# Kernel optimization log

Hardware: AMD Instinct MI355X
Metric: run time of the kernel (lower is better)

The kernel has to match this reference:

```python
import jax, jax.numpy as jnp
import numpy as np

B, T, V = 512, 200, 2048
E, H, I, A = 20, 100, 64, 32  # embedding, hidden, intermediate, actions


def setup_inputs() -> dict:
    key = jax.random.key(0)
    ks = jax.random.split(key, 12)
    batch = jax.random.uniform(ks[0], (B, T, V), dtype=jnp.float32)
    lengths = jax.random.randint(ks[1], (B,), 1, T + 1)
    s = 0.05
    W_emb = jax.random.normal(ks[2], (E, V), dtype=jnp.float32) * s
    b_emb = jnp.zeros((E,), jnp.float32)
    W_ih = jax.random.normal(ks[3], (4 * H, E), dtype=jnp.float32) * s
    W_hh = jax.random.normal(ks[4], (4 * H, H), dtype=jnp.float32) * s
    b_ih = jnp.zeros((4 * H,), jnp.float32)
    # torch init sets forget-gate bias (second quarter) to 1.0 in bias_hh
    b_hh = jnp.zeros((4 * H,), jnp.float32).at[H:2 * H].set(1.0)
    W1 = jax.random.normal(ks[5], (I, H), dtype=jnp.float32) * s
    b1 = jnp.zeros((I,), jnp.float32)
    W2 = jax.random.normal(ks[6], (A, I), dtype=jnp.float32) * s
    b2 = jnp.zeros((A,), jnp.float32)
    h0 = jnp.zeros((B, H), jnp.float32)
    c0 = jnp.zeros((B, H), jnp.float32)
    return {"batch": batch, "lengths": lengths, "W_emb": W_emb, "b_emb": b_emb,
            "W_ih": W_ih, "W_hh": W_hh, "b_ih": b_ih, "b_hh": b_hh,
            "W1": W1, "b1": b1, "W2": W2, "b2": b2, "h0": h0, "c0": c0}


def reference(batch, lengths, W_emb, b_emb, W_ih, W_hh, b_ih, b_hh,
              W1, b1, W2, b2, h0, c0):
    # Embedding via Linear: [B,T,V] @ [V,E] -> [B,T,E]
    emb = jnp.einsum('btv,ev->bte', batch, W_emb) + b_emb
    # Precompute input contribution to all gates: [B,T,4H]
    xg = jnp.einsum('bte,ge->btg', emb, W_ih) + b_ih + b_hh

    def step(carry, xg_t):
        h, c = carry
        gates = xg_t + h @ W_hh.T  # [B,4H]
        i, f, g, o = jnp.split(gates, 4, axis=-1)  # torch gate order i,f,g,o
        c = jax.nn.sigmoid(f) * c + jax.nn.sigmoid(i) * jnp.tanh(g)
        h = jax.nn.sigmoid(o) * jnp.tanh(c)
        return (h, c), h

    _, ys = jax.lax.scan(step, (h0, c0), jnp.swapaxes(xg, 0, 1))  # ys: [T,B,H]
    nb = batch.shape[0]
    h_final = ys[lengths - 1, jnp.arange(nb)]  # [B,H] output at last valid step
    inter = jax.nn.relu(h_final @ W1.T + b1)
    actions = inter @ W2.T + b2
    return actions
```

## Files before the change

### kernel.cpp

```cpp
#include <hip/hip_runtime.h>

#define BB 512
#define TT 200
#define VV 2048
#define EE 20
#define HH 100
#define G4 400
#define II 64
#define AA 32

typedef float vf2 __attribute__((ext_vector_type(2)));

#define WS_WT_OFF  1024
#define WS_EMB_OFF (1024 + VV * EE)

__global__ __launch_bounds__(512) void k0_prep(
    const int* __restrict__ lengths, const float* __restrict__ W_emb,
    int* __restrict__ off, float* __restrict__ Wt)
{
    if (blockIdx.x == 0) {
        __shared__ int s[BB];
        int tid = threadIdx.x;
        s[tid] = lengths[tid];
        __syncthreads();
        for (int d = 1; d < BB; d <<= 1) {
            int v = (tid >= d) ? s[tid - d] : 0;
            __syncthreads();
            if (tid >= d) s[tid] += v;
            __syncthreads();
        }
        off[tid + 1] = s[tid];
        if (tid == 0) off[0] = 0;
    } else {
        int idx = (blockIdx.x - 1) * 512 + threadIdx.x;
        if (idx < VV * EE) {
            int k = idx / EE, e = idx - k * EE;
            Wt[idx] = W_emb[(size_t)e * VV + k];
        }
    }
}

#define R1   128
#define KC   64
#define TSTR 68

__global__ __launch_bounds__(128) void k1_embed(
    const float* __restrict__ batch, const int* __restrict__ off,
    const float* __restrict__ Wt, const float* __restrict__ b_emb,
    float* __restrict__ emb)
{
    __shared__ float tile[R1 * TSTR];
    __shared__ float wch[(KC / 2) * EE * 2];
    __shared__ int   roff[R1];

    const int tid  = threadIdx.x;
    const int Nv   = off[BB];
    const int row0 = blockIdx.x * R1;
    if (row0 >= Nv) return;

    const int row    = row0 + tid;
    const bool active = row < Nv;

    int b = 0;
    {
        const int r = active ? row : 0;
        int lo = 0, hi = BB;
        while (lo + 1 < hi) {
            int mid = (lo + hi) >> 1;
            if (off[mid] <= r) lo = mid; else hi = mid;
        }
        b = lo;
    }
    const int t = (active ? row : 0) - off[b];
    roff[tid] = b * TT + t;
    __syncthreads();

    const float* srcp[16];
#pragma unroll
    for (int i = 0; i < 16; ++i) {
        int r = (tid >> 4) + 8 * i;
        srcp[i] = batch + (size_t)roff[r] * VV + (tid & 15) * 4;
    }

    vf2 acc[EE];
#pragma unroll
    for (int e = 0; e < EE; ++e) { acc[e].x = 0.f; acc[e].y = 0.f; }

#pragma unroll 1
    for (int c0 = 0; c0 < VV; c0 += KC) {
        __syncthreads();
#pragma unroll
        for (int i = 0; i < 16; ++i) {
            int r = (tid >> 4) + 8 * i;
            float4 v = *reinterpret_cast<const float4*>(srcp[i] + c0);
            *reinterpret_cast<float4*>(&tile[r * TSTR + (tid & 15) * 4]) = v;
        }
#pragma unroll
        for (int i = 0; i < 10; ++i) {
            int l = tid + i * 128;
            int k = l / EE, e = l - k * EE;
            wch[(k >> 1) * (2 * EE) + e * 2 + (k & 1)] = Wt[(size_t)c0 * EE + l];
        }
        __syncthreads();
#pragma unroll
        for (int p = 0; p < 16; ++p) {
            float4 xv = *reinterpret_cast<const float4*>(&tile[tid * TSTR + p * 4]);
            vf2 xlo, xhi;
            xlo.x = xv.x; xlo.y = xv.y;
            xhi.x = xv.z; xhi.y = xv.w;
            const float* wlo = &wch[(2 * p) * (2 * EE)];
            const float* whi = &wch[(2 * p + 1) * (2 * EE)];
#pragma unroll
            for (int e2 = 0; e2 < EE / 2; ++e2) {
                float4 wv = *reinterpret_cast<const float4*>(wlo + e2 * 4);
                vf2 w0, w1;
                w0.x = wv.x; w0.y = wv.y;
                w1.x = wv.z; w1.y = wv.w;
                acc[2 * e2]     = __builtin_elementwise_fma(w0, xlo, acc[2 * e2]);
                acc[2 * e2 + 1] = __builtin_elementwise_fma(w1, xlo, acc[2 * e2 + 1]);
            }
#pragma unroll
            for (int e2 = 0; e2 < EE / 2; ++e2) {
                float4 wv = *reinterpret_cast<const float4*>(whi + e2 * 4);
                vf2 w0, w1;
                w0.x = wv.x; w0.y = wv.y;
                w1.x = wv.z; w1.y = wv.w;
                acc[2 * e2]     = __builtin_elementwise_fma(w0, xhi, acc[2 * e2]);
                acc[2 * e2 + 1] = __builtin_elementwise_fma(w1, xhi, acc[2 * e2 + 1]);
            }
        }
    }

    if (active) {
        float o[EE];
#pragma unroll
        for (int e = 0; e < EE; ++e) o[e] = acc[e].x + acc[e].y + b_emb[e];
        float* dst = emb + (size_t)(b * TT + t) * EE;
#pragma unroll
        for (int e = 0; e < EE; e += 4)
            *reinterpret_cast<float4*>(dst + e) = make_float4(o[e], o[e+1], o[e+2], o[e+3]);
    }
}

__device__ __forceinline__ float fast_sig(float x) { return 1.f / (1.f + __expf(-x)); }
__device__ __forceinline__ float fast_tanh(float x) {
    x = fminf(fmaxf(x, -15.f), 15.f);
    float e = __expf(2.f * x);
    return (e - 1.f) / (e + 1.f);
}
__device__ __forceinline__ float dpp_xor1_add(float v) {
    int p = __builtin_amdgcn_update_dpp(0, __builtin_bit_cast(int, v), 0xB1, 0xF, 0xF, true);
    return v + __builtin_bit_cast(float, p);
}
__device__ __forceinline__ float dpp_xor2_add(float v) {
    int p = __builtin_amdgcn_update_dpp(0, __builtin_bit_cast(int, v), 0x4E, 0xF, 0xF, true);
    return v + __builtin_bit_cast(float, p);
}
#define QSTR 36

__global__ __launch_bounds__(448) void k2_lstm(
    const float* __restrict__ emb, const int* __restrict__ lengths,
    const float* __restrict__ W_ih, const float* __restrict__ W_hh,
    const float* __restrict__ b_ih, const float* __restrict__ b_hh,
    const float* __restrict__ W1, const float* __restrict__ b1,
    const float* __restrict__ W2, const float* __restrict__ b2,
    const float* __restrict__ h0, const float* __restrict__ c0,
    float* __restrict__ out)
{
    __shared__ float xhbuf[2][2][160];
    __shared__ float hfin[2][HH];
    __shared__ float inter[2][II];

    const int tid = threadIdx.x;
    const int b0  = blockIdx.x * 2;
    const int len0 = lengths[b0];
    const int len1 = lengths[b0 + 1];
    const int tmax = (len0 > len1) ? len0 : len1;

    const int j = tid >> 2, q = tid & 3;

    for (int i = tid; i < 2 * 2 * 160; i += 448) (&xhbuf[0][0][0])[i] = 0.f;

    vf2 w2[4][16];
    float biasv[4];
    float c_reg = 0.f;
    int lenq = 0;
    if (tid < G4) {
        const int rr[4] = { j, HH + j, 2 * HH + j, 3 * HH + j };
#pragma unroll
        for (int g = 0; g < 4; ++g) {
            const int r = rr[g];
#pragma unroll
            for (int mp = 0; mp < 16; ++mp) {
                int k = q * 32 + mp * 2;
                float2 v;
                if (k + 1 < EE)          v = *reinterpret_cast<const float2*>(&W_ih[r * EE + k]);
                else if (k + 1 < EE + HH) v = *reinterpret_cast<const float2*>(&W_hh[r * HH + k - EE]);
                else                     v = make_float2(0.f, 0.f);
                w2[g][mp].x = v.x; w2[g][mp].y = v.y;
            }
            biasv[g] = b_ih[r] + b_hh[r];
        }
        if (q < 2) c_reg = c0[(size_t)(b0 + q) * HH + j];
        lenq = (q == 0) ? len0 : len1;
    }
    __syncthreads();

    float xreg = 0.f;
    if (tid < G4) {
        if (q < 2) {
            int i = EE + j;
            xhbuf[0][q][(i >> 5) * QSTR + (i & 31)] = h0[(size_t)(b0 + q) * HH + j];
        }
    } else if (tid < G4 + 2 * EE) {
        const int wdx = tid - G4, bw = wdx / EE, e = wdx - bw * EE;
        const float* ep = emb + (size_t)(b0 + bw) * TT * EE;
        xhbuf[0][bw][e] = ep[e];
        xreg = ep[EE + e];
    }
    __syncthreads();

#pragma unroll 1
    for (int t = 0; t < tmax; ++t) {
        const int cur = t & 1, nxt = cur ^ 1;
        if (tid < G4) {
            vf2 a[4][2];
#pragma unroll
            for (int g = 0; g < 4; ++g) { a[g][0].x=0.f; a[g][0].y=0.f; a[g][1].x=0.f; a[g][1].y=0.f; }
            const float* xc = &xhbuf[cur][0][0];
#pragma unroll
            for (int m8 = 0; m8 < 8; ++m8) {
                float4 x0 = *reinterpret_cast<const float4*>(xc + q * QSTR + m8 * 4);
                float4 x1 = *reinterpret_cast<const float4*>(xc + 160 + q * QSTR + m8 * 4);
                vf2 xl0, xh0, xl1, xh1;
                xl0.x = x0.x; xl0.y = x0.y;  xh0.x = x0.z; xh0.y = x0.w;
                xl1.x = x1.x; xl1.y = x1.y;  xh1.x = x1.z; xh1.y = x1.w;
#pragma unroll
                for (int g = 0; g < 4; ++g) {
                    a[g][0] = __builtin_elementwise_fma(w2[g][2*m8],   xl0, a[g][0]);
                    a[g][0] = __builtin_elementwise_fma(w2[g][2*m8+1], xh0, a[g][0]);
                    a[g][1] = __builtin_elementwise_fma(w2[g][2*m8],   xl1, a[g][1]);
                    a[g][1] = __builtin_elementwise_fma(w2[g][2*m8+1], xh1, a[g][1]);
                }
            }
            float s_[4][2];
#pragma unroll
            for (int g = 0; g < 4; ++g) {
#pragma unroll
                for (int bb = 0; bb < 2; ++bb) {
                    float v = a[g][bb].x + a[g][bb].y;
                    v = dpp_xor1_add(v);
                    v = dpp_xor2_add(v);
                    s_[g][bb] = v;
                }
            }
            if (q < 2) {
                float gi = s_[0][q] + biasv[0];
                float gf = s_[1][q] + biasv[1];
                float gg = s_[2][q] + biasv[2];
                float go = s_[3][q] + biasv[3];
                c_reg = fast_sig(gf) * c_reg + fast_sig(gi) * fast_tanh(gg);
                float hv = fast_sig(go) * fast_tanh(c_reg);
                int i = EE + j;
                xhbuf[nxt][q][(i >> 5) * QSTR + (i & 31)] = hv;
                if (t == lenq - 1) hfin[q][j] = hv;
            }
        } else if (tid < G4 + 2 * EE) {
            const int wdx = tid - G4, bw = wdx / EE, e = wdx - bw * EE;
            xhbuf[nxt][bw][e] = xreg;
            xreg = (t + 2 < TT)
                 ? emb[((size_t)(b0 + bw) * TT + (t + 2)) * EE + e] : 0.f;
        }
        __syncthreads();
    }

    if (tid < 2 * II) {
        int bb = tid >> 6, i = tid & 63;
        float a = b1[i];
        const float* w1r = W1 + i * HH;
#pragma unroll
        for (int k = 0; k < HH; k += 4) {
            a += w1r[k] * hfin[bb][k] + w1r[k+1] * hfin[bb][k+1]
               + w1r[k+2] * hfin[bb][k+2] + w1r[k+3] * hfin[bb][k+3];
        }
        inter[bb][i] = fmaxf(a, 0.f);
    }
    __syncthreads();
    if (tid < 2 * AA) {
        int bb = tid >> 5, ai = tid & 31;
        float a = b2[ai];
        const float* w2r = W2 + ai * II;
#pragma unroll
        for (int k = 0; k < II; ++k) a += w2r[k] * inter[bb][k];
        out[(size_t)(b0 + bb) * AA + ai] = a;
    }
}

extern "C" void kernel_launch(void* const* d_in, const int* in_sizes, int n_in,
                              void* d_out, int out_size, void* d_ws, size_t ws_size,
                              hipStream_t stream) {
    const float* batch  = (const float*)d_in[0];
    const int*   lengths= (const int*)  d_in[1];
    const float* W_emb  = (const float*)d_in[2];
    const float* b_emb  = (const float*)d_in[3];
    const float* W_ih   = (const float*)d_in[4];
    const float* W_hh   = (const float*)d_in[5];
    const float* b_ih   = (const float*)d_in[6];
    const float* b_hh   = (const float*)d_in[7];
    const float* W1     = (const float*)d_in[8];
    const float* b1     = (const float*)d_in[9];
    const float* W2     = (const float*)d_in[10];
    const float* b2     = (const float*)d_in[11];
    const float* h0     = (const float*)d_in[12];
    const float* c0     = (const float*)d_in[13];
    float* out = (float*)d_out;

    int*   off = (int*)d_ws;
    float* Wt  = (float*)d_ws + WS_WT_OFF;
    float* emb = (float*)d_ws + WS_EMB_OFF;

    k0_prep<<<1 + (VV * EE + 511) / 512, 512, 0, stream>>>(lengths, W_emb, off, Wt);
    k1_embed<<<(BB * TT + R1 - 1) / R1, R1, 0, stream>>>(batch, off, Wt, b_emb, emb);
    k2_lstm<<<BB / 2, 448, 0, stream>>>(emb, lengths, W_ih, W_hh, b_ih, b_hh,
                                        W1, b1, W2, b2, h0, c0, out);
}
```

Baseline: 445.3 us.

## Prefetch embedding tiles into registers, stage emb in LDS, spread gate activations across lanes

The embedding GEMM now loads the next K-chunk of batch rows and weights into registers while the current chunk is computed, replacing the load-then-sync pattern with a software-pipelined double-buffer. The LSTM kernel copies each block's whole embedding sequence into shared memory up front, so the per-step global emb loads go away. The gate nonlinearities are spread so each of the four lanes per hidden unit evaluates one gate activation, with the results exchanged via DPP moves. This lowers the serial per-step transcendental latency. The cost is more registers in the GEMM kernel and about 32KB of extra LDS per LSTM block, which may reduce occupancy.

Result: slower. 508.1 us (+14.1%).

```diff
diff --git a/kernel.cpp b/kernel.cpp
--- a/kernel.cpp
+++ b/kernel.cpp
@@ -86,22 +86,35 @@
 #pragma unroll
     for (int e = 0; e < EE; ++e) { acc[e].x = 0.f; acc[e].y = 0.f; }
 
+    float4 xr[16];
+    float  wr[10];
+#pragma unroll
+    for (int i = 0; i < 16; ++i) xr[i] = *reinterpret_cast<const float4*>(srcp[i]);
+#pragma unroll
+    for (int i = 0; i < 10; ++i) wr[i] = Wt[tid + i * 128];
+
 #pragma unroll 1
     for (int c0 = 0; c0 < VV; c0 += KC) {
-        __syncthreads();
 #pragma unroll
         for (int i = 0; i < 16; ++i) {
             int r = (tid >> 4) + 8 * i;
-            float4 v = *reinterpret_cast<const float4*>(srcp[i] + c0);
-            *reinterpret_cast<float4*>(&tile[r * TSTR + (tid & 15) * 4]) = v;
+            *reinterpret_cast<float4*>(&tile[r * TSTR + (tid & 15) * 4]) = xr[i];
         }
 #pragma unroll
         for (int i = 0; i < 10; ++i) {
             int l = tid + i * 128;
             int k = l / EE, e = l - k * EE;
-            wch[(k >> 1) * (2 * EE) + e * 2 + (k & 1)] = Wt[(size_t)c0 * EE + l];
+            wch[(k >> 1) * (2 * EE) + e * 2 + (k & 1)] = wr[i];
         }
         __syncthreads();
+        if (c0 + KC < VV) {
+#pragma unroll
+            for (int i = 0; i < 16; ++i)
+                xr[i] = *reinterpret_cast<const float4*>(srcp[i] + c0 + KC);
+#pragma unroll
+            for (int i = 0; i < 10; ++i)
+                wr[i] = Wt[(size_t)(c0 + KC) * EE + tid + i * 128];
+        }
 #pragma unroll
         for (int p = 0; p < 16; ++p) {
             float4 xv = *reinterpret_cast<const float4*>(&tile[tid * TSTR + p * 4]);
@@ -129,6 +142,7 @@
                 acc[2 * e2 + 1] = __builtin_elementwise_fma(w1, xhi, acc[2 * e2 + 1]);
             }
         }
+        __syncthreads();
     }
 
     if (active) {
@@ -155,6 +169,11 @@
 __device__ __forceinline__ float dpp_xor2_add(float v) {
     int p = __builtin_amdgcn_update_dpp(0, __builtin_bit_cast(int, v), 0x4E, 0xF, 0xF, true);
     return v + __builtin_bit_cast(float, p);
+}
+template<int CTRL>
+__device__ __forceinline__ float dpp_mov(float v) {
+    int p = __builtin_amdgcn_update_dpp(0, __builtin_bit_cast(int, v), CTRL, 0xF, 0xF, true);
+    return __builtin_bit_cast(float, p);
 }
 #define QSTR 36
 
@@ -167,6 +186,7 @@
     const float* __restrict__ h0, const float* __restrict__ c0,
     float* __restrict__ out)
 {
+    __shared__ float emb_lds[2][TT][EE];
     __shared__ float xhbuf[2][2][160];
     __shared__ float hfin[2][HH];
     __shared__ float inter[2][II];
@@ -176,10 +196,14 @@
     const int len0 = lengths[b0];
     const int len1 = lengths[b0 + 1];
     const int tmax = (len0 > len1) ? len0 : len1;
-
     const int j = tid >> 2, q = tid & 3;
 
     for (int i = tid; i < 2 * 2 * 160; i += 448) (&xhbuf[0][0][0])[i] = 0.f;
+    {
+        const float4* srcp = reinterpret_cast<const float4*>(emb + (size_t)b0 * TT * EE);
+        float4* dst = reinterpret_cast<float4*>(&emb_lds[0][0][0]);
+        for (int i = tid; i < 2 * TT * EE / 4; i += 448) dst[i] = srcp[i];
+    }
 
     vf2 w2[4][16];
     float biasv[4];
@@ -206,7 +230,6 @@
     }
     __syncthreads();
 
-    float xreg = 0.f;
     if (tid < G4) {
         if (q < 2) {
             int i = EE + j;
@@ -214,9 +237,7 @@
         }
     } else if (tid < G4 + 2 * EE) {
         const int wdx = tid - G4, bw = wdx / EE, e = wdx - bw * EE;
-        const float* ep = emb + (size_t)(b0 + bw) * TT * EE;
-        xhbuf[0][bw][e] = ep[e];
-        xreg = ep[EE + e];
+        xhbuf[0][bw][e] = emb_lds[bw][0][e];
     }
     __syncthreads();
 
@@ -254,22 +275,28 @@
                     s_[g][bb] = v;
                 }
             }
+            float vq0 = (q==0) ? s_[0][0] : (q==1) ? s_[1][0] : (q==2) ? s_[2][0] : s_[3][0];
+            float vq1 = (q==0) ? s_[0][1] : (q==1) ? s_[1][1] : (q==2) ? s_[2][1] : s_[3][1];
+            float bq  = (q==0) ? biasv[0] : (q==1) ? biasv[1] : (q==2) ? biasv[2] : biasv[3];
+            vq0 += bq; vq1 += bq;
+            float nb0 = (q==2) ? fast_tanh(vq0) : fast_sig(vq0);
+            float nb1 = (q==2) ? fast_tanh(vq1) : fast_sig(vq1);
+            float p1_0 = dpp_mov<0xB1>(nb0), p2_0 = dpp_mov<0x4E>(nb0), p3_0 = dpp_mov<0x1B>(nb0);
+            float p1_1 = dpp_mov<0xB1>(nb1), p2_1 = dpp_mov<0x4E>(nb1), p3_1 = dpp_mov<0x1B>(nb1);
             if (q < 2) {
-                float gi = s_[0][q] + biasv[0];
-                float gf = s_[1][q] + biasv[1];
-                float gg = s_[2][q] + biasv[2];
-                float go = s_[3][q] + biasv[3];
-                c_reg = fast_sig(gf) * c_reg + fast_sig(gi) * fast_tanh(gg);
-                float hv = fast_sig(go) * fast_tanh(c_reg);
-                int i = EE + j;
-                xhbuf[nxt][q][(i >> 5) * QSTR + (i & 31)] = hv;
+                float ni = q ? p1_1 : nb0;
+                float nf = q ? nb1  : p1_0;
+                float ng = q ? p3_1 : p2_0;
+                float no = q ? p2_1 : p3_0;
+                c_reg = nf * c_reg + ni * ng;
+                float hv = no * fast_tanh(c_reg);
+                const int ii = EE + j;
+                xhbuf[nxt][q][(ii >> 5) * QSTR + (ii & 31)] = hv;
                 if (t == lenq - 1) hfin[q][j] = hv;
             }
         } else if (tid < G4 + 2 * EE) {
             const int wdx = tid - G4, bw = wdx / EE, e = wdx - bw * EE;
-            xhbuf[nxt][bw][e] = xreg;
-            xreg = (t + 2 < TT)
-                 ? emb[((size_t)(b0 + bw) * TT + (t + 2)) * EE + e] : 0.f;
+            if (t + 1 < tmax) xhbuf[nxt][bw][e] = emb_lds[bw][t + 1][e];
         }
         __syncthreads();
     }
```
